# Performance work log

Hardware: AMD Instinct MI355X
Metric: run time of the kernel (lower is better)

## Reference

```python
import jax, jax.numpy as jnp
import numpy as np
from jax import lax

B, CIN, H, W = 64, 3, 64, 64
HID = 128          # hidden_dim == embedding_dim
K = 1024           # num_embeddings
BETA = 0.25        # commitment cost


def _conv(x, w, b, stride):
    # torch Conv2d, padding=0, NCHW / OIHW weights
    y = lax.conv_general_dilated(x, w, (stride, stride), 'VALID',
                                 dimension_numbers=('NCHW', 'OIHW', 'NCHW'))
    return y + b[None, :, None, None]


def _conv_transpose(x, w, b, stride):
    # torch ConvTranspose2d, padding=0; w is [Cin, Cout, kh, kw] (torch layout)
    kh, kw = w.shape[2], w.shape[3]
    w2 = jnp.flip(w, (2, 3)).transpose(1, 0, 2, 3)  # -> OIHW, spatially flipped
    y = lax.conv_general_dilated(x, w2, (1, 1),
                                 [(kh - 1, kh - 1), (kw - 1, kw - 1)],
                                 lhs_dilation=(stride, stride),
                                 dimension_numbers=('NCHW', 'OIHW', 'NCHW'))
    return y + b[None, :, None, None]


def setup_inputs() -> dict:
    key = jax.random.key(0)
    ks = jax.random.split(key, 10)
    s = 0.05
    return {
        'x':      jax.random.normal(ks[0], (B, CIN, H, W), jnp.float32),
        'enc_w1': jax.random.normal(ks[1], (HID, CIN, 4, 4), jnp.float32) * s,
        'enc_b1': jnp.zeros((HID,), jnp.float32),
        'enc_w2': jax.random.normal(ks[2], (HID, HID, 2, 2), jnp.float32) * s,
        'enc_b2': jnp.zeros((HID,), jnp.float32),
        'codebook': jax.random.uniform(ks[3], (K, HID), jnp.float32,
                                       minval=-1.0 / K, maxval=1.0 / K),
        'dec_w1': jax.random.normal(ks[4], (HID, HID, 2, 2), jnp.float32) * s,
        'dec_b1': jnp.zeros((HID,), jnp.float32),
        'dec_w2': jax.random.normal(ks[5], (HID, CIN, 4, 4), jnp.float32) * s,
        'dec_b2': jnp.zeros((CIN,), jnp.float32),
    }


def reference(x, enc_w1, enc_b1, enc_w2, enc_b2, codebook,
              dec_w1, dec_b1, dec_w2, dec_b2):
    # ---- encoder ----
    z = jax.nn.relu(_conv(x, enc_w1, enc_b1, 2))
    z = jax.nn.relu(_conv(z, enc_w2, enc_b2, 1))   # [B, HID, 30, 30]

    # ---- vector quantizer (faithful to torch reshape semantics) ----
    D = HID
    flat = z.reshape(-1, D)                        # [N, D], C-order rows
    # squared euclidean distances (argmin identical to torch.cdist argmin)
    d2 = (jnp.sum(flat * flat, axis=1, keepdims=True)
          - 2.0 * flat @ codebook.T
          + jnp.sum(codebook * codebook, axis=1)[None, :])  # [N, K]
    idx = jnp.argmin(d2, axis=1)                   # [N]
    quantized = codebook[idx].reshape(z.shape)

    e_latent = jnp.mean((lax.stop_gradient(quantized) - z) ** 2)
    q_latent = jnp.mean((quantized - lax.stop_gradient(z)) ** 2)
    loss = q_latent + BETA * e_latent

    q_st = z + lax.stop_gradient(quantized - z)    # straight-through

    n = flat.shape[0]
    avg_probs = jnp.zeros((K,), z.dtype).at[idx].add(1.0) / n
    perplexity = jnp.exp(-jnp.sum(avg_probs * jnp.log(avg_probs + 1e-10)))

    # ---- decoder ----
    y = jax.nn.relu(_conv_transpose(q_st, dec_w1, dec_b1, 1))
    x_recon = _conv_transpose(y, dec_w2, dec_b2, 2)  # [B, 3, 64, 64]
    return x_recon, loss, perplexity
```

## Files before the change

kernel.cpp:

```cpp
#include <hip/hip_runtime.h>

#define B_    64
#define CIN_  3
#define HW_   64
#define HID_  128
#define K_    1024
#define H1_   31
#define H2_   30
#define NROWS_ 57600
#define NELEM_ 7372800

typedef __bf16 bf16_t;
typedef __attribute__((ext_vector_type(8))) __bf16 bf16x8;
typedef __attribute__((ext_vector_type(4))) float f32x4;
typedef __attribute__((ext_vector_type(16))) float f32x16;

__global__ __launch_bounds__(256) void wprep_k(const float* __restrict__ ew1,
    const float* __restrict__ ew2, const float* __restrict__ dw1,
    const float* __restrict__ dw2, const float* __restrict__ cb,
    bf16_t* __restrict__ wc1, bf16_t* __restrict__ wc2,
    bf16_t* __restrict__ wd1, bf16_t* __restrict__ wt2,
    bf16_t* __restrict__ cbb, float* __restrict__ cnorm,
    unsigned* __restrict__ hist, float* __restrict__ sse) {
  int id = blockIdx.x * 256 + threadIdx.x;
  int t = id >> 14, co = (id >> 7) & 127, ci = id & 127;
  wc2[id] = (bf16_t)ew2[(co * 128 + ci) * 4 + t];
  wd1[id] = (bf16_t)dw1[(ci * 128 + co) * 4 + (3 - t)];
  if (id < 8192) {
    int n = id >> 9, k = id & 511;
    int tap = k >> 7, c = k & 127;
    if (n < 12) {
      int nco = n >> 2, ph = (n >> 1) & 1, pw = n & 1;
      int off = (tap >> 1) * 8 + (tap & 1) * 2;
      wt2[id] = (bf16_t)dw2[c * 48 + nco * 16 + ph * 4 + pw + off];
    } else {
      wt2[id] = (bf16_t)0.f;
    }
    int c1 = id >> 6, k1 = id & 63;
    wc1[id] = (bf16_t)(k1 < 48 ? ew1[c1 * 48 + k1] : 0.f);
  }
  if (id < K_) {
    float s0 = 0.f;
    for (int d = 0; d < HID_; d += 4) {
      float4 v = *(const float4*)&cb[id * HID_ + d];
      bf16_t tt[4] = {(bf16_t)v.x, (bf16_t)v.y, (bf16_t)v.z, (bf16_t)v.w};
      *(ushort4*)&((ushort*)cbb)[id * HID_ + d] = *(ushort4*)tt;
      float f0 = (float)tt[0], f1 = (float)tt[1];
      float f2 = (float)tt[2], f3 = (float)tt[3];
      s0 += f0 * f0 + f1 * f1 + f2 * f2 + f3 * f3;
    }
    cnorm[id] = s0;
    hist[id] = 0u;
  }
  if (id == 0) *sse = 0.f;
}

__global__ __launch_bounds__(256, 2) void conv1m_k(const float* __restrict__ x,
    const bf16_t* __restrict__ wc1, const float* __restrict__ bias,
    ushort* __restrict__ z1t) {
  __shared__ __align__(16) bf16_t as_[64 * 72];
  __shared__ __align__(16) bf16_t bs_[128 * 72];
  int b = blockIdx.x >> 4, rt = blockIdx.x & 15;
  int tid = threadIdx.x, wv = tid >> 6, ln = tid & 63;
  const float* xb = x + (size_t)b * 12288;
  #pragma unroll
  for (int it = 0; it < 16; ++it) {
    int e = it * 256 + tid;
    int p = e >> 6, k = e & 63;
    float v = 0.f;
    if (k < 48) {
      int ci = k >> 4, kh = (k >> 2) & 3, kw = k & 3;
      int row = 2 * rt + (p >> 5); if (row > 30) row = 30;
      int col = p & 31;            if (col > 30) col = 30;
      v = xb[ci * 4096 + (2 * row + kh) * 64 + 2 * col + kw];
    }
    as_[p * 72 + k] = (bf16_t)v;
  }
  {
    const float4* wg = (const float4*)wc1;
    #pragma unroll
    for (int it = 0; it < 4; ++it) {
      int fi = it * 256 + tid;
      int co = fi >> 3, k8 = fi & 7;
      *(float4*)&bs_[co * 72 + k8 * 8] = wg[fi];
    }
  }
  __syncthreads();
  int q = ln >> 4, l = ln & 15;
  f32x4 acc8[8];
  #pragma unroll
  for (int c = 0; c < 8; ++c) acc8[c] = (f32x4){0.f, 0.f, 0.f, 0.f};
  bf16x8 af[2];
  #pragma unroll
  for (int kk = 0; kk < 2; ++kk)
    af[kk] = *(const bf16x8*)&as_[(wv * 16 + l) * 72 + kk * 32 + q * 8];
  #pragma unroll
  for (int cot = 0; cot < 8; ++cot) {
    #pragma unroll
    for (int kk = 0; kk < 2; ++kk) {
      bf16x8 bf = *(const bf16x8*)&bs_[(cot * 16 + l) * 72 + kk * 32 + q * 8];
      acc8[cot] = __builtin_amdgcn_mfma_f32_16x16x32_bf16(af[kk], bf,
                                                          acc8[cot], 0, 0, 0);
    }
  }
  #pragma unroll
  for (int cot = 0; cot < 8; ++cot) {
    int co = cot * 16 + l;
    float bv = bias[co];
    #pragma unroll
    for (int r = 0; r < 4; ++r) {
      int pos = wv * 16 + q * 4 + r;
      int prow = 2 * rt + (pos >> 5), pcol = pos & 31;
      if (prow < 31 && pcol < 31) {
        float v = fmaxf(acc8[cot][r] + bv, 0.f);
        bf16_t h = (bf16_t)v;
        z1t[((size_t)(b * 1024 + prow * 32 + pcol)) * 128 + co] = *(ushort*)&h;
      }
    }
  }
}

__global__ __launch_bounds__(256, 2) void conv2m_k(const bf16_t* __restrict__ z1t,
    const bf16_t* __restrict__ wc2, const float* __restrict__ bias,
    ushort* __restrict__ zbuf) {
  __shared__ __align__(16) bf16_t as_[98 * 136];
  __shared__ __align__(16) bf16_t bs_[128 * 136];
  int blk = blockIdx.x;
  int b = blk / 15, rt = blk % 15;
  int tid = threadIdx.x, wv = tid >> 6, ln = tid & 63;
  const float4* src = (const float4*)(z1t + ((size_t)b * 1024 + rt * 64) * 128);
  #pragma unroll
  for (int s = 0; s < 7; ++s) {
    int f = s * 256 + tid;
    if (f < 1568) {
      int lp = f >> 4, c16 = f & 15;
      *(float4*)&as_[lp * 136 + c16 * 8] = src[f];
    }
  }
  int m = wv * 16 + (ln & 15), q = ln >> 4;
  f32x4 acc8[8];
  #pragma unroll
  for (int c = 0; c < 8; ++c) acc8[c] = (f32x4){0.f, 0.f, 0.f, 0.f};
  const float4* w4 = (const float4*)wc2;
  #pragma unroll
  for (int t = 0; t < 4; ++t) {
    __syncthreads();
    #pragma unroll
    for (int s = 0; s < 8; ++s) {
      int f = s * 256 + tid;
      int co = f >> 4, c16 = f & 15;
      *(float4*)&bs_[co * 136 + c16 * 8] = w4[t * 2048 + f];
    }
    __syncthreads();
    int off = (t >> 1) * 32 + (t & 1);
    bf16x8 af[4];
    #pragma unroll
    for (int kk = 0; kk < 4; ++kk)
      af[kk] = *(const bf16x8*)&as_[(m + off) * 136 + kk * 32 + q * 8];
    #pragma unroll
    for (int cot = 0; cot < 8; ++cot) {
      #pragma unroll
      for (int kk = 0; kk < 4; ++kk) {
        bf16x8 bf = *(const bf16x8*)&bs_[(cot * 16 + (ln & 15)) * 136 +
                                         kk * 32 + q * 8];
        acc8[cot] = __builtin_amdgcn_mfma_f32_16x16x32_bf16(af[kk], bf,
                                                            acc8[cot], 0, 0, 0);
      }
    }
  }
  #pragma unroll
  for (int cot = 0; cot < 8; ++cot) {
    int co = cot * 16 + (ln & 15);
    float bv = bias[co];
    #pragma unroll
    for (int r = 0; r < 4; ++r) {
      int mo = wv * 16 + q * 4 + r;
      int ocol = mo & 31;
      if (ocol < 30) {
        int orow = rt * 2 + (mo >> 5);
        float v = fmaxf(acc8[cot][r] + bv, 0.f);
        bf16_t h = (bf16_t)v;
        zbuf[(size_t)(b * HID_ + co) * 900 + orow * 30 + ocol] = *(ushort*)&h;
      }
    }
  }
}

__global__ __launch_bounds__(256, 4) void vq1_k(const bf16_t* __restrict__ zb,
    const bf16_t* __restrict__ cbb, const float* __restrict__ cnorm,
    int* __restrict__ idxArr, unsigned* __restrict__ hist,
    float* __restrict__ sse) {
  __shared__ __align__(16) bf16_t cbs0[64 * 136];
  __shared__ __align__(16) bf16_t cbs1[64 * 136];
  __shared__ float cns[K_];
  __shared__ float redS[2][64];
  __shared__ int   redI[2][64];
  int n0 = blockIdx.x * 64;
  int tid = threadIdx.x;
  int wv = tid >> 6, ln = tid & 63;
  int lr = ln & 31, lh = ln >> 5;
  int mt = wv & 1, pt = wv >> 1;
  {
    float4 cv = ((const float4*)cnorm)[tid];
    cv.x *= -0.5f; cv.y *= -0.5f; cv.z *= -0.5f; cv.w *= -0.5f;
    ((float4*)cns)[tid] = cv;
  }
  const ushort* za = (const ushort*)zb +
                     ((size_t)(n0 + mt * 32 + lr)) * 128 + lh * 8;
  bf16x8 af[8];
  #pragma unroll
  for (int ks = 0; ks < 8; ++ks) af[ks] = *(const bf16x8*)(za + ks * 16);
  const float4* cg4 = (const float4*)cbb;
  float4 pf[4];
  #pragma unroll
  for (int s = 0; s < 4; ++s) pf[s] = cg4[s * 256 + tid];
  #pragma unroll
  for (int s = 0; s < 4; ++s) {
    int f = s * 256 + tid;
    *(float4*)&cbs0[(f >> 4) * 136 + (f & 15) * 8] = pf[s];
  }
  #pragma unroll
  for (int s = 0; s < 4; ++s)
    pf[s] = cg4[1024 + s * 256 + tid];
  float bS[16];
  int   bI[16];
  #pragma unroll
  for (int r = 0; r < 16; ++r) { bS[r] = -3.4e38f; bI[r] = 0; }
  int arow = (pt * 32 + lr) * 136 + lh * 8;
  __syncthreads();
  #pragma unroll 1
  for (int c = 0; c < 16; c += 2) {
    #pragma unroll
    for (int s = 0; s < 4; ++s) {
      int f = s * 256 + tid;
      *(float4*)&cbs1[(f >> 4) * 136 + (f & 15) * 8] = pf[s];
    }
    if (c + 2 < 16) {
      #pragma unroll
      for (int s = 0; s < 4; ++s)
        pf[s] = cg4[(c + 2) * 1024 + s * 256 + tid];
    }
    {
      int code = c * 64 + pt * 32 + lr;
      float hv = cns[code];
      f32x16 acc;
      #pragma unroll
      for (int r = 0; r < 16; ++r) acc[r] = hv;
      #pragma unroll
      for (int ks = 0; ks < 8; ++ks) {
        bf16x8 bfr = *(const bf16x8*)&cbs0[arow + ks * 16];
        acc = __builtin_amdgcn_mfma_f32_32x32x16_bf16(af[ks], bfr, acc,
                                                      0, 0, 0);
      }
      #pragma unroll
      for (int r = 0; r < 16; ++r)
        if (acc[r] > bS[r]) { bS[r] = acc[r]; bI[r] = code; }
    }
    __syncthreads();
    if (c + 2 < 16) {
      #pragma unroll
      for (int s = 0; s < 4; ++s) {
        int f = s * 256 + tid;
        *(float4*)&cbs0[(f >> 4) * 136 + (f & 15) * 8] = pf[s];
      }
    }
    if (c + 3 < 16) {
      #pragma unroll
      for (int s = 0; s < 4; ++s)
        pf[s] = cg4[(c + 3) * 1024 + s * 256 + tid];
    }
    {
      int code = (c + 1) * 64 + pt * 32 + lr;
      float hv = cns[code];
      f32x16 acc;
      #pragma unroll
      for (int r = 0; r < 16; ++r) acc[r] = hv;
      #pragma unroll
      for (int ks = 0; ks < 8; ++ks) {
        bf16x8 bfr = *(const bf16x8*)&cbs1[arow + ks * 16];
        acc = __builtin_amdgcn_mfma_f32_32x32x16_bf16(af[ks], bfr, acc,
                                                      0, 0, 0);
      }
      #pragma unroll
      for (int r = 0; r < 16; ++r)
        if (acc[r] > bS[r]) { bS[r] = acc[r]; bI[r] = code; }
    }
    __syncthreads();
  }
  #pragma unroll
  for (int r = 0; r < 16; ++r) {
    float s = bS[r]; int i = bI[r];
    #pragma unroll
    for (int o = 16; o > 0; o >>= 1) {
      float os = __shfl_xor(s, o, 64); int oi = __shfl_xor(i, o, 64);
      if (os > s || (os == s && oi < i)) { s = os; i = oi; }
    }
    bS[r] = s; bI[r] = i;
  }
  if (lr == 0) {
    #pragma unroll
    for (int r = 0; r < 16; ++r) {
      int row = (r & 3) + 8 * (r >> 2) + 4 * lh;
      redS[pt][mt * 32 + row] = bS[r];
      redI[pt][mt * 32 + row] = bI[r];
    }
  }
  __syncthreads();
  if (tid < 64) {
    float s0 = redS[0][tid], s1 = redS[1][tid];
    int i0 = redI[0][tid], i1 = redI[1][tid];
    bool t = (s1 > s0) || (s1 == s0 && i1 < i0);
    float sbest = t ? s1 : s0;
    int bi = t ? i1 : i0;
    idxArr[n0 + tid] = bi;
    atomicAdd(&hist[bi], 1u);
    const ushort* zr = (const ushort*)zb + (size_t)(n0 + tid) * 128;
    float zn = 0.f;
    #pragma unroll
    for (int sg = 0; sg < 16; ++sg) {
      bf16x8 v = *(const bf16x8*)(zr + sg * 8);
      #pragma unroll
      for (int e = 0; e < 8; ++e) {
        float fv = (float)v[e];
        zn = fmaf(fv, fv, zn);
      }
    }
    float se = zn - 2.f * sbest;
    #pragma unroll
    for (int o = 32; o > 0; o >>= 1) se += __shfl_down(se, o, 64);
    if (tid == 0) atomicAdd(sse, se);
  }
}

__global__ __launch_bounds__(256) void tqz_k(const bf16_t* __restrict__ cbb,
    const int* __restrict__ idxArr, ushort* __restrict__ qt) {
  __shared__ ushort t[60 * 128];
  int bid = blockIdx.x, tid = threadIdx.x;
  if (bid < 960) {
    int b = bid / 15, st = bid % 15;
    int s0 = st * 60;
    #pragma unroll
    for (int it = 0; it < 8; ++it) {
      int task = it * 256 + tid;
      if (task < 1920) {
        int sc = task >> 7, c = task & 127;
        int f = b * 115200 + c * 900 + s0 + sc * 4;
        int n = f >> 7, d = f & 127;
        int k = idxArr[n];
        ushort4 v = *(const ushort4*)((const ushort*)cbb + k * 128 + d);
        t[(sc * 4 + 0) * 128 + c] = v.x;
        t[(sc * 4 + 1) * 128 + c] = v.y;
        t[(sc * 4 + 2) * 128 + c] = v.z;
        t[(sc * 4 + 3) * 128 + c] = v.w;
      }
    }
    __syncthreads();
    #pragma unroll
    for (int it = 0; it < 4; ++it) {
      int task = it * 256 + tid;
      if (task < 960) {
        int sl = task >> 4, c16 = task & 15;
        int s = s0 + sl;
        int h = s / 30, w = s - h * 30;
        int p = (h + 1) * 32 + (w + 1);
        *(uint4*)&qt[((size_t)(b * 1024 + p)) * 128 + c16 * 8] =
            *(uint4*)&t[sl * 128 + c16 * 8];
      }
    }
  } else {
    int zb_ = (bid - 960) * 4;
    uint4 zz = {0u, 0u, 0u, 0u};
    for (int e = tid; e < 4 * 124 * 16; e += 256) {
      int bb = zb_ + e / (124 * 16);
      int rem = e % (124 * 16);
      int pe = rem >> 4, s16 = rem & 15;
      int p;
      if (pe < 32) p = pe;
      else if (pe < 64) p = 31 * 32 + (pe - 32);
      else {
        int idx = pe - 64;
        p = (1 + (idx >> 1)) * 32 + ((idx & 1) ? 31 : 0);
      }
      *(uint4*)&qt[((size_t)(bb * 1024 + p)) * 128 + s16 * 8] = zz;
    }
  }
}

__global__ __launch_bounds__(256, 2) void convt1m_k(const bf16_t* __restrict__ qt,
    const bf16_t* __restrict__ wd1, const float* __restrict__ bias,
    ushort* __restrict__ yt) {
  __shared__ __align__(16) bf16_t as_[98 * 136];
  __shared__ __align__(16) bf16_t bs_[128 * 136];
  int blk = blockIdx.x;
  int b = blk >> 4, rt = blk & 15;
  int tid = threadIdx.x, wv = tid >> 6, ln = tid & 63;
  {
    uint4 zz = {0u, 0u, 0u, 0u};
    ushort* ytb = yt + (size_t)b * 1156 * 128;
    int nrows = (rt < 15) ? 2 : 1;
    int r0 = 2 * rt + 1;
    for (int e = tid; e < nrows * 48; e += 256) {
      int rr = e / 48, rem = e % 48, cc = rem / 16, s16 = rem % 16;
      int col = (cc == 0) ? 0 : (cc == 1 ? 32 : 33);
      *(uint4*)&ytb[((size_t)((r0 + rr) * 34 + col)) * 128 + s16 * 8] = zz;
    }
    if (rt == 0)
      for (int e = tid; e < 34 * 16; e += 256)
        *(uint4*)&ytb[((size_t)(e >> 4)) * 128 + (e & 15) * 8] = zz;
    if (rt == 15)
      for (int e = tid; e < 2 * 34 * 16; e += 256) {
        int rr = 32 + e / 544, rem = e % 544;
        *(uint4*)&ytb[((size_t)(rr * 34 + (rem >> 4))) * 128 + (rem & 15) * 8]
            = zz;
      }
  }
  const float4* src = (const float4*)(qt + (size_t)b * 1024 * 128);
  #pragma unroll
  for (int s = 0; s < 7; ++s) {
    int f = s * 256 + tid;
    if (f < 1568) {
      int lp = f >> 4, c16 = f & 15;
      int gr = rt * 64 + lp;
      if (gr > 1023) gr = 1023;
      *(float4*)&as_[lp * 136 + c16 * 8] = src[gr * 16 + c16];
    }
  }
  int m = wv * 16 + (ln & 15), q = ln >> 4;
  f32x4 acc8[8];
  #pragma unroll
  for (int c = 0; c < 8; ++c) acc8[c] = (f32x4){0.f, 0.f, 0.f, 0.f};
  const float4* w4 = (const float4*)wd1;
  #pragma unroll
  for (int t = 0; t < 4; ++t) {
    __syncthreads();
    #pragma unroll
    for (int s = 0; s < 8; ++s) {
      int f = s * 256 + tid;
      int co = f >> 4, c16 = f & 15;
      *(float4*)&bs_[co * 136 + c16 * 8] = w4[t * 2048 + f];
    }
    __syncthreads();
    int off = (t >> 1) * 32 + (t & 1);
    bf16x8 af[4];
    #pragma unroll
    for (int kk = 0; kk < 4; ++kk)
      af[kk] = *(const bf16x8*)&as_[(m + off) * 136 + kk * 32 + q * 8];
    #pragma unroll
    for (int cot = 0; cot < 8; ++cot) {
      #pragma unroll
      for (int kk = 0; kk < 4; ++kk) {
        bf16x8 bf = *(const bf16x8*)&bs_[(cot * 16 + (ln & 15)) * 136 +
                                         kk * 32 + q * 8];
        acc8[cot] = __builtin_amdgcn_mfma_f32_16x16x32_bf16(af[kk], bf,
                                                            acc8[cot], 0, 0, 0);
      }
    }
  }
  #pragma unroll
  for (int cot = 0; cot < 8; ++cot) {
    int co = cot * 16 + (ln & 15);
    float bv = bias[co];
    #pragma unroll
    for (int r = 0; r < 4; ++r) {
      int mo = wv * 16 + q * 4 + r;
      int orow = rt * 2 + (mo >> 5), ocol = mo & 31;
      if (orow < 31 && ocol < 31) {
        float v = fmaxf(acc8[cot][r] + bv, 0.f);
        bf16_t h = (bf16_t)v;
        yt[((size_t)b * 1156 + (orow + 1) * 34 + (ocol + 1)) * 128 + co] =
            *(ushort*)&h;
      }
    }
  }
}

__global__ __launch_bounds__(256, 2) void convt2m_k(const bf16_t* __restrict__ yt,
    const bf16_t* __restrict__ wt2, const float* __restrict__ bias,
    const unsigned* __restrict__ hist, const float* __restrict__ sse,
    float* __restrict__ out) {
  __shared__ __align__(16) bf16_t as_[128 * 136];
  __shared__ float redf[256];
  int b = blockIdx.x >> 4, rt = blockIdx.x & 15;
  int tid = threadIdx.x, wv = tid >> 6, ln = tid & 63;
  const float4* src = (const float4*)(yt + ((size_t)b * 1156 + rt * 68) * 128);
  #pragma unroll
  for (int s = 0; s < 8; ++s) {
    int f = s * 256 + tid;
    int lp = f >> 4, c16 = f & 15;
    *(float4*)&as_[lp * 136 + c16 * 8] = src[f];
  }
  __syncthreads();
  int mloc = wv * 16 + (ln & 15), q = ln >> 4;
  int qh = mloc >> 5, qw = mloc & 31;
  int base = (qh + 1) * 34 + qw + 1;
  f32x4 acc = {0.f, 0.f, 0.f, 0.f};
  #pragma unroll
  for (int kc = 0; kc < 16; ++kc) {
    int tap = kc >> 2;
    int toff = (tap & 1) + (tap >> 1) * 34;
    bf16x8 af = *(const bf16x8*)&as_[(base - toff) * 136 +
                                     (kc & 3) * 32 + q * 8];
    bf16x8 bf = *(const bf16x8*)&wt2[(size_t)(ln & 15) * 512 + kc * 32 + q * 8];
    acc = __builtin_amdgcn_mfma_f32_16x16x32_bf16(af, bf, acc, 0, 0, 0);
  }
  __syncthreads();
  float* bb = (float*)as_;
  #pragma unroll
  for (int r = 0; r < 4; ++r)
    bb[(wv * 16 + q * 4 + r) * 16 + (ln & 15)] = acc[r];
  __syncthreads();
  if (tid < 192) {
    int row_id = tid >> 4;
    int co = row_id >> 2, ohoff = row_id & 3;
    int qhl = ohoff >> 1, ph = ohoff & 1;
    float bv = bias[co];
    int ow0 = (tid & 15) * 4;
    float tmp[4];
    #pragma unroll
    for (int e = 0; e < 4; ++e) {
      int ow = ow0 + e;
      tmp[e] = bb[(qhl * 32 + (ow >> 1)) * 16 + co * 4 + ph * 2 + (ow & 1)]
               + bv;
    }
    *(float4*)&out[((size_t)(b * 3 + co)) * 4096 + (rt * 4 + ohoff) * 64 + ow0]
        = *(float4*)tmp;
  }
  if (blockIdx.x == 0) {
    float e = 0.f;
    for (int k = tid; k < K_; k += 256) {
      float p = (float)hist[k] * (1.0f / (float)NROWS_);
      e += p * logf(p + 1e-10f);
    }
    redf[tid] = e;
    __syncthreads();
    #pragma unroll
    for (int t = 128; t > 0; t >>= 1) {
      if (tid < t) redf[tid] += redf[tid + t];
      __syncthreads();
    }
    if (tid == 0) {
      out[786432] = 1.25f * (*sse) * (1.0f / (float)NELEM_);
      out[786433] = expf(-redf[0]);
    }
  }
}

extern "C" void kernel_launch(void* const* d_in, const int* in_sizes, int n_in,
                              void* d_out, int out_size, void* d_ws,
                              size_t ws_size, hipStream_t stream) {
  (void)in_sizes; (void)n_in; (void)out_size; (void)ws_size;
  const float* x   = (const float*)d_in[0];
  const float* ew1 = (const float*)d_in[1];
  const float* eb1 = (const float*)d_in[2];
  const float* ew2 = (const float*)d_in[3];
  const float* eb2 = (const float*)d_in[4];
  const float* cb  = (const float*)d_in[5];
  const float* dw1 = (const float*)d_in[6];
  const float* db1 = (const float*)d_in[7];
  const float* dw2 = (const float*)d_in[8];
  const float* db2 = (const float*)d_in[9];
  float* out = (float*)d_out;
  char* ws = (char*)d_ws;

  ushort*   yt    = (ushort*)(ws);
  bf16_t*   z1t   = (bf16_t*)(ws + 65175552);
  bf16_t*   qt    = (bf16_t*)(ws + 65175552);
  ushort*   zbuf  = (ushort*)(ws + 81985536);
  bf16_t*   cbb   = (bf16_t*)(ws + 96731136);
  bf16_t*   wc2   = (bf16_t*)(ws + 96993280);
  bf16_t*   wd1   = (bf16_t*)(ws + 97124352);
  int*      idxArr= (int*)(ws + 97255424);
  unsigned* hist  = (unsigned*)(ws + 97485824);
  float*    cnorm = (float*)(ws + 97489920);
  float*    sse   = (float*)(ws + 97494016);
  bf16_t*   wt2   = (bf16_t*)(ws + 97497088);
  bf16_t*   wc1   = (bf16_t*)(ws + 97513472);

  wprep_k<<<dim3(256), dim3(256), 0, stream>>>(ew1, ew2, dw1, dw2, cb,
                                               wc1, wc2, wd1, wt2,
                                               cbb, cnorm, hist, sse);
  conv1m_k<<<dim3(1024), dim3(256), 0, stream>>>(x, wc1, eb1, (ushort*)z1t);
  conv2m_k<<<dim3(960), dim3(256), 0, stream>>>(z1t, wc2, eb2, zbuf);
  vq1_k<<<dim3(900), dim3(256), 0, stream>>>((const bf16_t*)zbuf, cbb, cnorm,
                                             idxArr, hist, sse);
  tqz_k<<<dim3(976), dim3(256), 0, stream>>>(cbb, idxArr, (ushort*)qt);
  convt1m_k<<<dim3(1024), dim3(256), 0, stream>>>(qt, wd1, db1, yt);
  convt2m_k<<<dim3(1024), dim3(256), 0, stream>>>((const bf16_t*)yt, wt2, db2,
                                                  hist, sse, out);
}
```

Before: 260.0 us.

## Stage VQ codebook tiles via direct global-to-LDS loads with XOR swizzle

Replaces the register-staged codebook prefetch in the VQ argmin kernel with global_load_lds direct-to-LDS copies into a double buffer. A source-side XOR swizzle replaces the padded 136-stride layout to avoid LDS bank conflicts. The occupancy hint is lowered from 4 to 2 waves per SIMD. This frees the prefetch registers and VALU store work, but it depends on the async loads finishing before the barrier and on the swizzle matching exactly on both the write and read sides.

```diff
diff --git a/kernel.cpp b/kernel.cpp
--- a/kernel.cpp
+++ b/kernel.cpp
@@ -14,6 +14,12 @@
 typedef __attribute__((ext_vector_type(8))) __bf16 bf16x8;
 typedef __attribute__((ext_vector_type(4))) float f32x4;
 typedef __attribute__((ext_vector_type(16))) float f32x16;
+
+__device__ __forceinline__ void gload_lds16(const void* g, void* l) {
+  __builtin_amdgcn_global_load_lds(
+      (const __attribute__((address_space(1))) unsigned int*)g,
+      (__attribute__((address_space(3))) unsigned int*)l, 16, 0, 0);
+}
 
 __global__ __launch_bounds__(256) void wprep_k(const float* __restrict__ ew1,
     const float* __restrict__ ew2, const float* __restrict__ dw1,
@@ -186,12 +192,11 @@
   }
 }
 
-__global__ __launch_bounds__(256, 4) void vq1_k(const bf16_t* __restrict__ zb,
+__global__ __launch_bounds__(256, 2) void vq1_k(const bf16_t* __restrict__ zb,
     const bf16_t* __restrict__ cbb, const float* __restrict__ cnorm,
     int* __restrict__ idxArr, unsigned* __restrict__ hist,
     float* __restrict__ sse) {
-  __shared__ __align__(16) bf16_t cbs0[64 * 136];
-  __shared__ __align__(16) bf16_t cbs1[64 * 136];
+  __shared__ __align__(16) bf16_t cbs[2][64 * 128];
   __shared__ float cns[K_];
   __shared__ float redS[2][64];
   __shared__ int   redI[2][64];
@@ -200,6 +205,22 @@
   int wv = tid >> 6, ln = tid & 63;
   int lr = ln & 31, lh = ln >> 5;
   int mt = wv & 1, pt = wv >> 1;
+  int rr = pt * 32 + lr;
+  const char* cbBase = (const char*)cbb;
+
+#define STAGE_(buf, c)                                                       \
+  {                                                                          \
+    const char* gsrc_ = cbBase + (size_t)(c) * 16384;                        \
+    char* lb_ = (char*)&cbs[buf][0] + (tid >> 6) * 1024;                     \
+    _Pragma("unroll")                                                        \
+    for (int i_ = 0; i_ < 4; ++i_) {                                         \
+      int D_ = i_ * 4096 + tid * 16;                                         \
+      int so_ = D_ ^ (((D_ >> 8) & 15) << 4);                                \
+      gload_lds16(gsrc_ + so_, lb_ + i_ * 4096);                             \
+    }                                                                        \
+  }
+
+  STAGE_(0, 0);
   {
     float4 cv = ((const float4*)cnorm)[tid];
     cv.x *= -0.5f; cv.y *= -0.5f; cv.z *= -0.5f; cv.w *= -0.5f;
@@ -210,82 +231,43 @@
   bf16x8 af[8];
   #pragma unroll
   for (int ks = 0; ks < 8; ++ks) af[ks] = *(const bf16x8*)(za + ks * 16);
-  const float4* cg4 = (const float4*)cbb;
-  float4 pf[4];
-  #pragma unroll
-  for (int s = 0; s < 4; ++s) pf[s] = cg4[s * 256 + tid];
-  #pragma unroll
-  for (int s = 0; s < 4; ++s) {
-    int f = s * 256 + tid;
-    *(float4*)&cbs0[(f >> 4) * 136 + (f & 15) * 8] = pf[s];
-  }
-  #pragma unroll
-  for (int s = 0; s < 4; ++s)
-    pf[s] = cg4[1024 + s * 256 + tid];
+  int off8[8];
+  #pragma unroll
+  for (int ks = 0; ks < 8; ++ks)
+    off8[ks] = rr * 256 + ((lh * 16 + ks * 32) ^ ((rr & 15) << 4));
   float bS[16];
   int   bI[16];
   #pragma unroll
   for (int r = 0; r < 16; ++r) { bS[r] = -3.4e38f; bI[r] = 0; }
-  int arow = (pt * 32 + lr) * 136 + lh * 8;
+
+#define COMPUTE_(buf, c)                                                     \
+  {                                                                          \
+    int code_ = (c) * 64 + rr;                                               \
+    float hv_ = cns[code_];                                                  \
+    f32x16 acc_;                                                             \
+    _Pragma("unroll")                                                        \
+    for (int r_ = 0; r_ < 16; ++r_) acc_[r_] = hv_;                          \
+    _Pragma("unroll")                                                        \
+    for (int ks_ = 0; ks_ < 8; ++ks_) {                                      \
+      bf16x8 bfr_ = *(const bf16x8*)((const char*)&cbs[buf][0] + off8[ks_]); \
+      acc_ = __builtin_amdgcn_mfma_f32_32x32x16_bf16(af[ks_], bfr_, acc_,    \
+                                                     0, 0, 0);               \
+    }                                                                        \
+    _Pragma("unroll")                                                        \
+    for (int r_ = 0; r_ < 16; ++r_)                                          \
+      if (acc_[r_] > bS[r_]) { bS[r_] = acc_[r_]; bI[r_] = code_; }          \
+  }
+
   __syncthreads();
+  STAGE_(1, 1);
   #pragma unroll 1
   for (int c = 0; c < 16; c += 2) {
-    #pragma unroll
-    for (int s = 0; s < 4; ++s) {
-      int f = s * 256 + tid;
-      *(float4*)&cbs1[(f >> 4) * 136 + (f & 15) * 8] = pf[s];
-    }
-    if (c + 2 < 16) {
-      #pragma unroll
-      for (int s = 0; s < 4; ++s)
-        pf[s] = cg4[(c + 2) * 1024 + s * 256 + tid];
-    }
-    {
-      int code = c * 64 + pt * 32 + lr;
-      float hv = cns[code];
-      f32x16 acc;
-      #pragma unroll
-      for (int r = 0; r < 16; ++r) acc[r] = hv;
-      #pragma unroll
-      for (int ks = 0; ks < 8; ++ks) {
-        bf16x8 bfr = *(const bf16x8*)&cbs0[arow + ks * 16];
-        acc = __builtin_amdgcn_mfma_f32_32x32x16_bf16(af[ks], bfr, acc,
-                                                      0, 0, 0);
-      }
-      #pragma unroll
-      for (int r = 0; r < 16; ++r)
-        if (acc[r] > bS[r]) { bS[r] = acc[r]; bI[r] = code; }
-    }
-    __syncthreads();
-    if (c + 2 < 16) {
-      #pragma unroll
-      for (int s = 0; s < 4; ++s) {
-        int f = s * 256 + tid;
-        *(float4*)&cbs0[(f >> 4) * 136 + (f & 15) * 8] = pf[s];
-      }
-    }
-    if (c + 3 < 16) {
-      #pragma unroll
-      for (int s = 0; s < 4; ++s)
-        pf[s] = cg4[(c + 3) * 1024 + s * 256 + tid];
-    }
-    {
-      int code = (c + 1) * 64 + pt * 32 + lr;
-      float hv = cns[code];
-      f32x16 acc;
-      #pragma unroll
-      for (int r = 0; r < 16; ++r) acc[r] = hv;
-      #pragma unroll
-      for (int ks = 0; ks < 8; ++ks) {
-        bf16x8 bfr = *(const bf16x8*)&cbs1[arow + ks * 16];
-        acc = __builtin_amdgcn_mfma_f32_32x32x16_bf16(af[ks], bfr, acc,
-                                                      0, 0, 0);
-      }
-      #pragma unroll
-      for (int r = 0; r < 16; ++r)
-        if (acc[r] > bS[r]) { bS[r] = acc[r]; bI[r] = code; }
-    }
-    __syncthreads();
+    COMPUTE_(0, c);
+    __syncthreads();
+    if (c + 2 < 16) STAGE_(0, c + 2);
+    COMPUTE_(1, c + 1);
+    __syncthreads();
+    if (c + 3 < 16) STAGE_(1, c + 3);
   }
   #pragma unroll
   for (int r = 0; r < 16; ++r) {
@@ -330,6 +312,8 @@
     for (int o = 32; o > 0; o >>= 1) se += __shfl_down(se, o, 64);
     if (tid == 0) atomicAdd(sse, se);
   }
+#undef STAGE_
+#undef COMPUTE_
 }
 
 __global__ __launch_bounds__(256) void tqz_k(const bf16_t* __restrict__ cbb,
```

New measurement: 238.5 us. 1.09x faster.
